# Optimization experiments

Measured on AMD Instinct MI355X. Metric: run time of the kernel, lower is better.

The kernel has to match this reference:

```python
import jax, jax.numpy as jnp
import numpy as np


def setup_inputs() -> dict:
    key = jax.random.key(0)
    k1, k2, k3 = jax.random.split(key, 3)
    B, N, M = 64, 1024, 1024
    src = jax.random.normal(k1, (B, 3, N), dtype=jnp.float32)
    tgt = jax.random.normal(k2, (B, 3, M), dtype=jnp.float32)
    scores = jax.random.normal(k3, (B, N, M), dtype=jnp.float32)
    return {"src": src, "tgt": tgt, "scores": scores}


def reference(src, tgt, scores):
    # softmax over the tgt-point axis (dim=2 in torch)
    p = jax.nn.softmax(scores, axis=2)                       # [B,N,M]
    # src_corr = tgt @ scores^T  -> soft correspondences in tgt for each src point
    src_corr = jnp.einsum('bdm,bnm->bdn', tgt, p)            # [B,3,N]
    src_mean = src.mean(axis=2, keepdims=True)               # [B,3,1]
    corr_mean = src_corr.mean(axis=2, keepdims=True)         # [B,3,1]
    src_c = src - src_mean
    corr_c = src_corr - corr_mean
    # cross-covariance H = src_centered @ src_corr_centered^T  -> [B,3,3]
    H = jnp.einsum('bdn,ben->bde', src_c, corr_c)
    U, S, Vh = jnp.linalg.svd(H)                             # batched 3x3 SVD
    V = jnp.swapaxes(Vh, -1, -2)
    Ut = jnp.swapaxes(U, -1, -2)
    R0 = V @ Ut                                              # candidate rotation
    det = jnp.linalg.det(R0)                                 # [B]
    # reflection fix: flip last column of V where det < 0 (reflect = diag(1,1,-1))
    flip = jnp.where(det < 0, -1.0, 1.0)                     # [B]
    ones = jnp.ones_like(flip)
    col_scale = jnp.stack([ones, ones, flip], axis=-1)[:, None, :]  # [B,1,3]
    R = (V * col_scale) @ Ut                                 # [B,3,3]
    t = (-R @ src_mean) + corr_mean                          # [B,3,1]
    return R, t.reshape(src.shape[0], 3)
```

## Files before the change

### kernel.cpp

```cpp
#include <hip/hip_runtime.h>
#include <math.h>

#define BATCH 64
#define NPTS  1024
#define MPTS  1024
#define BLOCKS_PER_BATCH 8
#define WAVES_PER_BLOCK  8
#define ROWS_PER_WAVE    16

typedef float f32x4 __attribute__((ext_vector_type(4)));

__global__ __launch_bounds__(512, 4) void softmax_stats_kernel(
    const float* __restrict__ src,
    const float* __restrict__ tgt,
    const float* __restrict__ scores,
    float* __restrict__ partials)
{
    __shared__ float tgt_lds[3 * MPTS];
    __shared__ float src_lds[3][BLOCKS_PER_BATCH * 16];
    __shared__ float part[WAVES_PER_BLOCK][16];

    const int tid  = threadIdx.x;
    const int lane = tid & 63;
    const int wave = tid >> 6;
    const int b    = blockIdx.x >> 3;
    const int bb   = blockIdx.x & 7;
    const int nrows_blk = NPTS / BLOCKS_PER_BATCH;
    const int n_base    = bb * nrows_blk;
    const int n_wave    = n_base + wave * ROWS_PER_WAVE;

    const f32x4* tgt_g = (const f32x4*)(tgt + (size_t)b * 3 * MPTS);
    f32x4* tgt_l = (f32x4*)tgt_lds;

    const float* srow0 = scores + ((size_t)b * NPTS + n_wave) * MPTS;
    f32x4 va[4], vb[4];
    #pragma unroll
    for (int k = 0; k < 4; ++k)
        va[k] = __builtin_nontemporal_load((const f32x4*)srow0 + k * 64 + lane);

    {
        int i0 = tid, i1 = tid + 512;
        tgt_l[i0] = tgt_g[i0];
        if (i1 < 768) tgt_l[i1] = tgt_g[i1];
        if (tid < 384) {
            int d = tid >> 7, nn = tid & 127;
            src_lds[d][nn] = src[((size_t)b * 3 + d) * NPTS + n_base + nn];
        }
    }
    __syncthreads();

    float st[15];
    #pragma unroll
    for (int i = 0; i < 15; ++i) st[i] = 0.f;

    const f32x4* t0p = (const f32x4*)(tgt_lds + 0 * MPTS);
    const f32x4* t1p = (const f32x4*)(tgt_lds + 1 * MPTS);
    const f32x4* t2p = (const f32x4*)(tgt_lds + 2 * MPTS);

    auto process = [&](const f32x4 v[4], int rr) {
        float sum = 0.f, w0 = 0.f, w1 = 0.f, w2 = 0.f;
        #pragma unroll
        for (int k = 0; k < 4; ++k) {
            const int m4 = k * 64 + lane;
            float e0 = __expf(v[k].x);
            float e1 = __expf(v[k].y);
            float e2 = __expf(v[k].z);
            float e3 = __expf(v[k].w);
            sum += e0 + e1 + e2 + e3;
            f32x4 t0 = t0p[m4], t1 = t1p[m4], t2 = t2p[m4];
            w0 += e0 * t0.x + e1 * t0.y + e2 * t0.z + e3 * t0.w;
            w1 += e0 * t1.x + e1 * t1.y + e2 * t1.z + e3 * t1.w;
            w2 += e0 * t2.x + e1 * t2.y + e2 * t2.z + e3 * t2.w;
        }
        #pragma unroll
        for (int off = 32; off >= 1; off >>= 1) {
            sum += __shfl_xor(sum, off);
            w0  += __shfl_xor(w0, off);
            w1  += __shfl_xor(w1, off);
            w2  += __shfl_xor(w2, off);
        }
        const float inv = 1.0f / sum;
        const float c0 = w0 * inv, c1 = w1 * inv, c2 = w2 * inv;
        const int ln = wave * ROWS_PER_WAVE + rr;
        const float s0 = src_lds[0][ln], s1 = src_lds[1][ln], s2 = src_lds[2][ln];
        st[0] += s0; st[1] += s1; st[2] += s2;
        st[3] += c0; st[4] += c1; st[5] += c2;
        st[6]  += s0 * c0; st[7]  += s0 * c1; st[8]  += s0 * c2;
        st[9]  += s1 * c0; st[10] += s1 * c1; st[11] += s1 * c2;
        st[12] += s2 * c0; st[13] += s2 * c1; st[14] += s2 * c2;
    };

    const float* srow_base = scores + ((size_t)b * NPTS + n_wave) * MPTS;
    for (int r = 0; r < ROWS_PER_WAVE; r += 2) {
        const f32x4* rp1 = (const f32x4*)(srow_base + (size_t)(r + 1) * MPTS);
        #pragma unroll
        for (int k = 0; k < 4; ++k)
            vb[k] = __builtin_nontemporal_load(rp1 + k * 64 + lane);
        process(va, r);
        if (r + 2 < ROWS_PER_WAVE) {
            const f32x4* rp2 = (const f32x4*)(srow_base + (size_t)(r + 2) * MPTS);
            #pragma unroll
            for (int k = 0; k < 4; ++k)
                va[k] = __builtin_nontemporal_load(rp2 + k * 64 + lane);
        }
        process(vb, r + 1);
    }

    if (lane == 0) {
        #pragma unroll
        for (int i = 0; i < 15; ++i) part[wave][i] = st[i];
        part[wave][15] = 0.f;
    }
    __syncthreads();

    if (tid < 16) {
        float a = 0.f;
        #pragma unroll
        for (int w = 0; w < WAVES_PER_BLOCK; ++w) a += part[w][tid];
        partials[(size_t)blockIdx.x * 16 + tid] = a;
    }
}

__global__ __launch_bounds__(64) void procrustes_kernel(
    const float* __restrict__ partials,
    float* __restrict__ out)
{
    const int b    = blockIdx.x;
    const int lane = threadIdx.x;

    float red = partials[(size_t)b * 128 + lane]
              + partials[(size_t)b * 128 + 64 + lane];
    red += __shfl_xor(red, 16);
    red += __shfl_xor(red, 32);
    float a[15];
    #pragma unroll
    for (int i = 0; i < 15; ++i) a[i] = __shfl(red, i);

    if (lane == 0) {
        const float invN = 1.0f / (float)NPTS;
        float mus[3], muc[3];
        #pragma unroll
        for (int d = 0; d < 3; ++d) { mus[d] = a[d] * invN; muc[d] = a[3 + d] * invN; }

        float Hm[3][3];
        #pragma unroll
        for (int d = 0; d < 3; ++d)
            #pragma unroll
            for (int e = 0; e < 3; ++e)
                Hm[d][e] = a[6 + d * 3 + e] - (float)NPTS * mus[d] * muc[e];

        float Bm[3][3], Vm[3][3];
        #pragma unroll
        for (int i = 0; i < 3; ++i)
            #pragma unroll
            for (int j = 0; j < 3; ++j) {
                Bm[i][j] = Hm[i][j];
                Vm[i][j] = (i == j) ? 1.f : 0.f;
            }

        const int PP[3] = {0, 0, 1};
        const int QQ[3] = {1, 2, 2};
        for (int sweep = 0; sweep < 8; ++sweep) {
            for (int rr = 0; rr < 3; ++rr) {
                const int p = PP[rr], q = QQ[rr];
                float aa = 0.f, bb = 0.f, c = 0.f;
                #pragma unroll
                for (int i = 0; i < 3; ++i) {
                    aa += Bm[i][p] * Bm[i][p];
                    bb += Bm[i][q] * Bm[i][q];
                    c  += Bm[i][p] * Bm[i][q];
                }
                if (fabsf(c) <= 1e-12f * sqrtf(aa * bb) || c == 0.f) continue;
                float tau = (bb - aa) / (2.f * c);
                float tt  = copysignf(1.f, tau) / (fabsf(tau) + sqrtf(1.f + tau * tau));
                float cs  = 1.f / sqrtf(1.f + tt * tt);
                float sn  = cs * tt;
                #pragma unroll
                for (int i = 0; i < 3; ++i) {
                    float bp = Bm[i][p], bq = Bm[i][q];
                    Bm[i][p] = cs * bp - sn * bq;
                    Bm[i][q] = sn * bp + cs * bq;
                    float vp = Vm[i][p], vq = Vm[i][q];
                    Vm[i][p] = cs * vp - sn * vq;
                    Vm[i][q] = sn * vp + cs * vq;
                }
            }
        }

        float sig[3];
        #pragma unroll
        for (int j = 0; j < 3; ++j)
            sig[j] = sqrtf(Bm[0][j] * Bm[0][j] + Bm[1][j] * Bm[1][j] + Bm[2][j] * Bm[2][j]);

        const int SP[3] = {0, 1, 0};
        const int SQ[3] = {1, 2, 1};
        for (int rr = 0; rr < 3; ++rr) {
            int p = SP[rr], q = SQ[rr];
            if (sig[p] < sig[q]) {
                float tsw = sig[p]; sig[p] = sig[q]; sig[q] = tsw;
                #pragma unroll
                for (int i = 0; i < 3; ++i) {
                    float t1 = Bm[i][p]; Bm[i][p] = Bm[i][q]; Bm[i][q] = t1;
                    float t2 = Vm[i][p]; Vm[i][p] = Vm[i][q]; Vm[i][q] = t2;
                }
            }
        }

        float Um[3][3];
        #pragma unroll
        for (int j = 0; j < 2; ++j) {
            float inv = 1.f / fmaxf(sig[j], 1e-30f);
            #pragma unroll
            for (int i = 0; i < 3; ++i) Um[i][j] = Bm[i][j] * inv;
        }
        if (sig[2] > 1e-6f * fmaxf(sig[0], 1e-30f)) {
            float inv = 1.f / sig[2];
            #pragma unroll
            for (int i = 0; i < 3; ++i) Um[i][2] = Bm[i][2] * inv;
        } else {
            float cx = Um[1][0] * Um[2][1] - Um[2][0] * Um[1][1];
            float cy = Um[2][0] * Um[0][1] - Um[0][0] * Um[2][1];
            float cz = Um[0][0] * Um[1][1] - Um[1][0] * Um[0][1];
            float inv = 1.f / fmaxf(sqrtf(cx * cx + cy * cy + cz * cz), 1e-30f);
            Um[0][2] = cx * inv; Um[1][2] = cy * inv; Um[2][2] = cz * inv;
        }

        float detU = Um[0][0] * (Um[1][1] * Um[2][2] - Um[1][2] * Um[2][1])
                   - Um[0][1] * (Um[1][0] * Um[2][2] - Um[1][2] * Um[2][0])
                   + Um[0][2] * (Um[1][0] * Um[2][1] - Um[1][1] * Um[2][0]);
        float detV = Vm[0][0] * (Vm[1][1] * Vm[2][2] - Vm[1][2] * Vm[2][1])
                   - Vm[0][1] * (Vm[1][0] * Vm[2][2] - Vm[1][2] * Vm[2][0])
                   + Vm[0][2] * (Vm[1][0] * Vm[2][1] - Vm[1][1] * Vm[2][0]);
        float flip = (detU * detV < 0.f) ? -1.f : 1.f;
        float fl[3] = {1.f, 1.f, flip};

        float R[3][3];
        #pragma unroll
        for (int i = 0; i < 3; ++i)
            #pragma unroll
            for (int j = 0; j < 3; ++j)
                R[i][j] = Vm[i][0] * fl[0] * Um[j][0]
                        + Vm[i][1] * fl[1] * Um[j][1]
                        + Vm[i][2] * fl[2] * Um[j][2];

        float* Rout = out + (size_t)b * 9;
        #pragma unroll
        for (int i = 0; i < 3; ++i)
            #pragma unroll
            for (int j = 0; j < 3; ++j)
                Rout[i * 3 + j] = R[i][j];

        float* tout = out + (size_t)BATCH * 9 + (size_t)b * 3;
        #pragma unroll
        for (int i = 0; i < 3; ++i)
            tout[i] = muc[i] - (R[i][0] * mus[0] + R[i][1] * mus[1] + R[i][2] * mus[2]);
    }
}

extern "C" void kernel_launch(void* const* d_in, const int* in_sizes, int n_in,
                              void* d_out, int out_size, void* d_ws, size_t ws_size,
                              hipStream_t stream) {
    const float* src    = (const float*)d_in[0];
    const float* tgt    = (const float*)d_in[1];
    const float* scores = (const float*)d_in[2];
    float* out      = (float*)d_out;
    float* partials = (float*)d_ws;

    softmax_stats_kernel<<<dim3(BATCH * BLOCKS_PER_BATCH), dim3(512), 0, stream>>>(
        src, tgt, scores, partials);

    procrustes_kernel<<<dim3(BATCH), dim3(64), 0, stream>>>(partials, out);
}
```

Baseline: 66.00 us.

## Split batches across more blocks and keep tgt in registers instead of LDS

Work is split across 32 blocks per batch with 4 rows per wave, instead of 8 blocks with 16 rows per wave, so the grid has more blocks to fill the GPU. The tgt and src LDS staging and its __syncthreads are dropped. Each lane holds its slice of tgt in registers and reads src values straight from global memory. The cost is more redundant tgt loads per block and more partials for the second kernel to reduce, which now sums 8 values per lane.

```diff
diff --git a/kernel.cpp b/kernel.cpp
--- a/kernel.cpp
+++ b/kernel.cpp
@@ -4,9 +4,10 @@
 #define BATCH 64
 #define NPTS  1024
 #define MPTS  1024
-#define BLOCKS_PER_BATCH 8
-#define WAVES_PER_BLOCK  8
-#define ROWS_PER_WAVE    16
+#define WAVES_PER_BLOCK 8
+#define ROWS_PER_WAVE   4
+#define BLOCKS_PER_BATCH 32
+#define NBLOCKS (BATCH * BLOCKS_PER_BATCH)
 
 typedef float f32x4 __attribute__((ext_vector_type(4)));
 
@@ -16,61 +17,44 @@
     const float* __restrict__ scores,
     float* __restrict__ partials)
 {
-    __shared__ float tgt_lds[3 * MPTS];
-    __shared__ float src_lds[3][BLOCKS_PER_BATCH * 16];
     __shared__ float part[WAVES_PER_BLOCK][16];
 
     const int tid  = threadIdx.x;
     const int lane = tid & 63;
     const int wave = tid >> 6;
-    const int b    = blockIdx.x >> 3;
-    const int bb   = blockIdx.x & 7;
-    const int nrows_blk = NPTS / BLOCKS_PER_BATCH;
-    const int n_base    = bb * nrows_blk;
-    const int n_wave    = n_base + wave * ROWS_PER_WAVE;
-
-    const f32x4* tgt_g = (const f32x4*)(tgt + (size_t)b * 3 * MPTS);
-    f32x4* tgt_l = (f32x4*)tgt_lds;
-
-    const float* srow0 = scores + ((size_t)b * NPTS + n_wave) * MPTS;
+    const int b    = blockIdx.x >> 5;
+    const int bb   = blockIdx.x & 31;
+    const int n0   = bb * 32 + wave * ROWS_PER_WAVE;
+
+    const float* srow_base = scores + ((size_t)b * NPTS + n0) * MPTS;
     f32x4 va[4], vb[4];
     #pragma unroll
     for (int k = 0; k < 4; ++k)
-        va[k] = __builtin_nontemporal_load((const f32x4*)srow0 + k * 64 + lane);
-
-    {
-        int i0 = tid, i1 = tid + 512;
-        tgt_l[i0] = tgt_g[i0];
-        if (i1 < 768) tgt_l[i1] = tgt_g[i1];
-        if (tid < 384) {
-            int d = tid >> 7, nn = tid & 127;
-            src_lds[d][nn] = src[((size_t)b * 3 + d) * NPTS + n_base + nn];
-        }
-    }
-    __syncthreads();
+        va[k] = __builtin_nontemporal_load((const f32x4*)srow_base + k * 64 + lane);
+
+    f32x4 tg[3][4];
+    #pragma unroll
+    for (int d = 0; d < 3; ++d)
+        #pragma unroll
+        for (int k = 0; k < 4; ++k)
+            tg[d][k] = *((const f32x4*)(tgt + ((size_t)b * 3 + d) * MPTS) + k * 64 + lane);
 
     float st[15];
     #pragma unroll
     for (int i = 0; i < 15; ++i) st[i] = 0.f;
 
-    const f32x4* t0p = (const f32x4*)(tgt_lds + 0 * MPTS);
-    const f32x4* t1p = (const f32x4*)(tgt_lds + 1 * MPTS);
-    const f32x4* t2p = (const f32x4*)(tgt_lds + 2 * MPTS);
-
-    auto process = [&](const f32x4 v[4], int rr) {
+    auto process = [&](const f32x4 v[4], int r) {
         float sum = 0.f, w0 = 0.f, w1 = 0.f, w2 = 0.f;
         #pragma unroll
         for (int k = 0; k < 4; ++k) {
-            const int m4 = k * 64 + lane;
             float e0 = __expf(v[k].x);
             float e1 = __expf(v[k].y);
             float e2 = __expf(v[k].z);
             float e3 = __expf(v[k].w);
             sum += e0 + e1 + e2 + e3;
-            f32x4 t0 = t0p[m4], t1 = t1p[m4], t2 = t2p[m4];
-            w0 += e0 * t0.x + e1 * t0.y + e2 * t0.z + e3 * t0.w;
-            w1 += e0 * t1.x + e1 * t1.y + e2 * t1.z + e3 * t1.w;
-            w2 += e0 * t2.x + e1 * t2.y + e2 * t2.z + e3 * t2.w;
+            w0 += e0 * tg[0][k].x + e1 * tg[0][k].y + e2 * tg[0][k].z + e3 * tg[0][k].w;
+            w1 += e0 * tg[1][k].x + e1 * tg[1][k].y + e2 * tg[1][k].z + e3 * tg[1][k].w;
+            w2 += e0 * tg[2][k].x + e1 * tg[2][k].y + e2 * tg[2][k].z + e3 * tg[2][k].w;
         }
         #pragma unroll
         for (int off = 32; off >= 1; off >>= 1) {
@@ -81,8 +65,10 @@
         }
         const float inv = 1.0f / sum;
         const float c0 = w0 * inv, c1 = w1 * inv, c2 = w2 * inv;
-        const int ln = wave * ROWS_PER_WAVE + rr;
-        const float s0 = src_lds[0][ln], s1 = src_lds[1][ln], s2 = src_lds[2][ln];
+        const int n = n0 + r;
+        const float s0 = src[((size_t)b * 3 + 0) * NPTS + n];
+        const float s1 = src[((size_t)b * 3 + 1) * NPTS + n];
+        const float s2 = src[((size_t)b * 3 + 2) * NPTS + n];
         st[0] += s0; st[1] += s1; st[2] += s2;
         st[3] += c0; st[4] += c1; st[5] += c2;
         st[6]  += s0 * c0; st[7]  += s0 * c1; st[8]  += s0 * c2;
@@ -90,20 +76,25 @@
         st[12] += s2 * c0; st[13] += s2 * c1; st[14] += s2 * c2;
     };
 
-    const float* srow_base = scores + ((size_t)b * NPTS + n_wave) * MPTS;
-    for (int r = 0; r < ROWS_PER_WAVE; r += 2) {
-        const f32x4* rp1 = (const f32x4*)(srow_base + (size_t)(r + 1) * MPTS);
-        #pragma unroll
-        for (int k = 0; k < 4; ++k)
-            vb[k] = __builtin_nontemporal_load(rp1 + k * 64 + lane);
-        process(va, r);
-        if (r + 2 < ROWS_PER_WAVE) {
-            const f32x4* rp2 = (const f32x4*)(srow_base + (size_t)(r + 2) * MPTS);
-            #pragma unroll
-            for (int k = 0; k < 4; ++k)
-                va[k] = __builtin_nontemporal_load(rp2 + k * 64 + lane);
-        }
-        process(vb, r + 1);
+    {
+        const f32x4* r1p = (const f32x4*)(srow_base + 1 * MPTS);
+        #pragma unroll
+        for (int k = 0; k < 4; ++k)
+            vb[k] = __builtin_nontemporal_load(r1p + k * 64 + lane);
+        process(va, 0);
+
+        const f32x4* r2p = (const f32x4*)(srow_base + 2 * MPTS);
+        #pragma unroll
+        for (int k = 0; k < 4; ++k)
+            va[k] = __builtin_nontemporal_load(r2p + k * 64 + lane);
+        process(vb, 1);
+
+        const f32x4* r3p = (const f32x4*)(srow_base + 3 * MPTS);
+        #pragma unroll
+        for (int k = 0; k < 4; ++k)
+            vb[k] = __builtin_nontemporal_load(r3p + k * 64 + lane);
+        process(va, 2);
+        process(vb, 3);
     }
 
     if (lane == 0) {
@@ -128,8 +119,10 @@
     const int b    = blockIdx.x;
     const int lane = threadIdx.x;
 
-    float red = partials[(size_t)b * 128 + lane]
-              + partials[(size_t)b * 128 + 64 + lane];
+    float red = 0.f;
+    #pragma unroll
+    for (int j = 0; j < 8; ++j)
+        red += partials[(size_t)b * 512 + j * 64 + lane];
     red += __shfl_xor(red, 16);
     red += __shfl_xor(red, 32);
     float a[15];
@@ -266,7 +259,7 @@
     float* out      = (float*)d_out;
     float* partials = (float*)d_ws;
 
-    softmax_stats_kernel<<<dim3(BATCH * BLOCKS_PER_BATCH), dim3(512), 0, stream>>>(
+    softmax_stats_kernel<<<dim3(NBLOCKS), dim3(512), 0, stream>>>(
         src, tgt, scores, partials);
 
     procrustes_kernel<<<dim3(BATCH), dim3(64), 0, stream>>>(partials, out);
```

Result: slower. 112.6 us (+70.6%).
